# Kernel optimization log

Hardware: AMD Instinct MI355X
Metric: run time of the kernel (lower is better)

Reference implementation:

```python
import jax, jax.numpy as jnp
import numpy as np

H = 200
W = 200
SH = 2.0  # h / h_meters = 200/100
SW = 2.0
THRESH = 0.05   # opacity prune threshold
CHUNK = 128     # gaussians per scan step
EPS_T = 1e-4    # 3DGS transmittance early-stop
ALPHA_MIN = 1.0 / 255.0


def _rasterize(means3D, colors, opac, cov3D):
    """Orthographic BEV 3D-Gaussian-splat rasterization for one sample.
    means3D (N,3), colors (N,d), opac (N,1), cov3D (N,6) packed [xx,xy,xz,yy,yz,zz].
    Returns (d, H, W) image. Depth is identically 0 under the BEV view matrix,
    so compositing order is the input order (stable), matching the CUDA sort.
    """
    N, d = colors.shape
    P = H * W
    # pixel centers, row-major flatten: p = y*W + x
    gy, gx = jnp.meshgrid(jnp.arange(H, dtype=jnp.float32),
                          jnp.arange(W, dtype=jnp.float32), indexing='ij')
    pxf = gx.reshape(-1)
    pyf = gy.reshape(-1)

    # project means with full_proj_transform: u = -sh*y + H/2, v = -sw*x + W/2
    u = -SH * means3D[:, 1] + H / 2.0
    v = -SW * means3D[:, 0] + W / 2.0

    # 2D covariance: W2 @ Cov3D @ W2^T + 0.3*I with W2 = [[0,sh,0],[sw,0,0]]
    a = SH * SH * cov3D[:, 3] + 0.3   # var along image x (from Sigma_yy)
    c = SW * SW * cov3D[:, 0] + 0.3   # var along image y (from Sigma_xx)
    b = SH * SW * cov3D[:, 1]
    det = a * c - b * b
    valid = det > 0.0
    det_s = jnp.where(valid, det, 1.0)
    conA = c / det_s
    conB = b / det_s   # power uses +conB*dx*dy (conic.y = -b/det in CUDA)
    conC = a / det_s

    # fold pruning mask (opacity threshold) and validity into opacity
    op = jnp.where((opac[:, 0] > THRESH) & valid, opac[:, 0], 0.0)

    K = N // CHUNK
    chunks = tuple(t.reshape(K, CHUNK, *t.shape[1:])
                   for t in (u, v, conA, conB, conC, op, colors))

    def body(carry, ch):
        img, T = carry  # img (P,d), T (P,)
        u_, v_, A_, B_, C_, op_, col_ = ch
        dx = u_[:, None] - pxf[None, :]          # (C,P)
        dy = v_[:, None] - pyf[None, :]
        power = -0.5 * (A_[:, None] * dx * dx + C_[:, None] * dy * dy) \
                + B_[:, None] * dx * dy
        alpha = jnp.minimum(0.99, op_[:, None] * jnp.exp(jnp.minimum(power, 0.0)))
        # CUDA skips power>0 and alpha < 1/255
        alpha = jnp.where((power > 0.0) | (alpha < ALPHA_MIN), 0.0, alpha)
        # early termination: skip gaussian i (and all after) once T would drop < 1e-4
        T_incl = T[None, :] * jnp.cumprod(1.0 - alpha, axis=0)
        alpha = jnp.where(T_incl < EPS_T, 0.0, alpha)
        cp = jnp.cumprod(1.0 - alpha, axis=0)    # inclusive products
        T_excl = jnp.concatenate([jnp.ones((1, P), dtype=cp.dtype), cp[:-1]], axis=0)
        wgt = alpha * T_excl * T[None, :]        # (C,P)
        img = img + jnp.einsum('cp,cd->pd', wgt, col_)
        T = T * cp[-1]
        return (img, T), None

    img0 = jnp.zeros((P, d), dtype=colors.dtype)
    T0 = jnp.ones((P,), dtype=colors.dtype)
    (img, T), _ = jax.lax.scan(body, (img0, T0), chunks)
    # background is zeros -> no bg term; reshape to (d, H, W)
    return img.reshape(H, W, d).transpose(2, 0, 1)


def setup_inputs() -> dict:
    key = jax.random.key(0)
    k1, k2, k3, k4 = jax.random.split(key, 4)
    B, N, D = 2, 1024, 32
    features = jax.random.normal(k1, (B, N, D), dtype=jnp.float32)
    # BEV covers +/-50m; scale positions so most gaussians land on the canvas
    means3D = jax.random.normal(k2, (B, N, 3), dtype=jnp.float32) * 20.0
    cov3D = jax.random.uniform(k3, (B, N, 6), dtype=jnp.float32)
    opacities = jax.random.uniform(k4, (B, N, 1), dtype=jnp.float32)
    return {"features": features, "means3D": means3D,
            "cov3D": cov3D, "opacities": opacities}


def reference(features, means3D, cov3D, opacities):
    bev = jax.vmap(_rasterize)(means3D, features, opacities, cov3D)  # (B,d,H,W)
    mask = opacities[..., 0] > THRESH
    mean_count = mask.astype(jnp.float32).sum(axis=1).mean()
    return bev, mean_count
```

## Files before the change

kernel.cpp:

```cpp
#include <hip/hip_runtime.h>


#define HH 200
#define WW 200
#define DD 32
#define NG 1024
#define BB 2
#define TOTG (BB*NG)
#define OUT_IMG (BB*DD*HH*WW)


__global__ __launch_bounds__(256) void prepass_kernel(
    const float* __restrict__ means,
    const float* __restrict__ cov,
    const float* __restrict__ opac,
    float* __restrict__ ws,
    float* __restrict__ out)
{
    const int g = blockIdx.x * 256 + threadIdx.x;
    if (g < TOTG) {
        float o   = opac[g];
        float cxx = cov[g*6+0], cxy = cov[g*6+1], cyy = cov[g*6+3];
        float a   = 4.f*cyy + 0.3f;
        float cc  = 4.f*cxx + 0.3f;
        float bb  = 4.f*cxy;
        float det = a*cc - bb*bb;
        float u=0.f, v=0.f, A=0.f, Bc=0.f, Cc=0.f, pl=0.f, r=-1.f;
        if (o > 0.05f && det > 0.f) {
            float inv = 1.f/det;
            A = cc*inv; Bc = bb*inv; Cc = a*inv;
            float mx = means[g*3+0], my = means[g*3+1];
            u = -2.f*my + 100.f;
            v = -2.f*mx + 100.f;
            pl = -__logf(255.f*o);
            float qmax = -2.f*pl;
            float htr = 0.5f*(A+Cc), hdf = 0.5f*(A-Cc);
            float lmin = htr - sqrtf(hdf*hdf + Bc*Bc);
            r = sqrtf(qmax/lmin) + 0.5f;
        }
        ws[0*TOTG+g]=u;  ws[1*TOTG+g]=v;  ws[2*TOTG+g]=A;  ws[3*TOTG+g]=Bc;
        ws[4*TOTG+g]=Cc; ws[5*TOTG+g]=o;  ws[6*TOTG+g]=pl; ws[7*TOTG+g]=r;
    }
    if (blockIdx.x == 0) {
        const int tid = threadIdx.x;
        float s = 0.f;
        for (int i = tid; i < TOTG; i += 256)
            s += (opac[i] > 0.05f) ? 1.f : 0.f;
#pragma unroll
        for (int off = 32; off > 0; off >>= 1)
            s += __shfl_down(s, off, 64);
        __shared__ float wsum[4];
        if ((tid & 63) == 0) wsum[tid >> 6] = s;
        __syncthreads();
        if (tid == 0)
            out[OUT_IMG] = (wsum[0]+wsum[1]+wsum[2]+wsum[3]) / (float)BB;
    }
}

__global__ __launch_bounds__(64) void render_kernel(
    const float* __restrict__ feats,
    const float* __restrict__ ws,
    float* __restrict__ out)
{
    __shared__ float su[64], sv[64], sA[64], sB[64], sC[64], sop[64], spl[64];
    __shared__ int   sg[64];

    const int b    = blockIdx.z;
    const int lane = threadIdx.x;
    const int px   = blockIdx.x*8 + (lane & 7);
    const int py   = blockIdx.y*8 + (lane >> 3);
    const float pxf = (float)px, pyf = (float)py;
    const float cx  = blockIdx.x*8 + 3.5f;
    const float cy  = blockIdx.y*8 + 3.5f;

    const float* __restrict__ featsB = feats + (size_t)b * NG * DD;
    const int gbase = b * NG;

    float4 acc[8];
#pragma unroll
    for (int j = 0; j < 8; ++j) acc[j] = make_float4(0.f,0.f,0.f,0.f);
    float T = 1.f, P = 1.f;
    bool skip = false;

    for (int k = 0; k < NG/64; ++k) {
        const int g = gbase + k*64 + lane;
        const float u = ws[0*TOTG+g];
        const float v = ws[1*TOTG+g];
        const float r = ws[7*TOTG+g];
        const bool flag = (r > 0.f) &&
                          (fabsf(u - cx) <= 3.5f + r) &&
                          (fabsf(v - cy) <= 3.5f + r);
        const unsigned long long mask = __ballot(flag);
        const int m = (int)__popcll(mask);
        __syncthreads();
        if (flag) {
            const int pos = (int)__popcll(mask & ((1ull << lane) - 1ull));
            su[pos]=u; sv[pos]=v;
            sA[pos]=ws[2*TOTG+g]; sB[pos]=ws[3*TOTG+g]; sC[pos]=ws[4*TOTG+g];
            sop[pos]=ws[5*TOTG+g]; spl[pos]=ws[6*TOTG+g];
            sg[pos]=k*64 + lane;
        }
        __syncthreads();

        if (!skip) {
            for (int i = 0; i < m; ++i) {
                const float dx = su[i] - pxf;
                const float dy = sv[i] - pyf;
                const float pw = fmaf(sB[i], dx*dy,
                                      -0.5f*(sA[i]*dx*dx + sC[i]*dy*dy));
                if (pw > 0.f) continue;
                if (pw < spl[i] - 1e-3f) continue;
                const float alpha = fminf(0.99f, sop[i] * __expf(pw));
                if (alpha < (1.f/255.f)) continue;
                const float om = 1.f - alpha;
                const float tp = T * P;
                if (tp * om < 1e-4f) { skip = true; break; }
                const float w = alpha * tp;
                const float4* __restrict__ col =
                    (const float4*)(featsB + (size_t)sg[i] * DD);
#pragma unroll
                for (int j = 0; j < 8; ++j) {
                    const float4 c4 = col[j];
                    acc[j].x = fmaf(w, c4.x, acc[j].x);
                    acc[j].y = fmaf(w, c4.y, acc[j].y);
                    acc[j].z = fmaf(w, c4.z, acc[j].z);
                    acc[j].w = fmaf(w, c4.w, acc[j].w);
                }
                P *= om;
            }
        }
        if (k & 1) {
            T *= P; P = 1.f; skip = false;
            if (__ballot(T >= 1e-4f) == 0ull) break;
        }
    }

    const size_t base = (size_t)b * DD * (HH*WW) + (size_t)py * WW + px;
#pragma unroll
    for (int j = 0; j < 8; ++j) {
        out[base + (size_t)(4*j+0)*(HH*WW)] = acc[j].x;
        out[base + (size_t)(4*j+1)*(HH*WW)] = acc[j].y;
        out[base + (size_t)(4*j+2)*(HH*WW)] = acc[j].z;
        out[base + (size_t)(4*j+3)*(HH*WW)] = acc[j].w;
    }
}

extern "C" void kernel_launch(void* const* d_in, const int* in_sizes, int n_in,
                              void* d_out, int out_size, void* d_ws, size_t ws_size,
                              hipStream_t stream) {
    const float* feats = (const float*)d_in[0];
    const float* means = (const float*)d_in[1];
    const float* cvr   = (const float*)d_in[2];
    const float* opc   = (const float*)d_in[3];
    float* out = (float*)d_out;
    float* wsf = (float*)d_ws;

    prepass_kernel<<<dim3(TOTG/256), dim3(256), 0, stream>>>(means, cvr, opc, wsf, out);
    render_kernel<<<dim3(WW/8, HH/8, BB), dim3(64), 0, stream>>>(feats, wsf, out);
}
```

Measured before the change: 86.54 us.

## Split gaussian list across four waves per tile and fuse prepass into render

```diff
diff --git a/kernel.cpp b/kernel.cpp
--- a/kernel.cpp
+++ b/kernel.cpp
@@ -6,67 +6,29 @@
 #define DD 32
 #define NG 1024
 #define BB 2
-#define TOTG (BB*NG)
 #define OUT_IMG (BB*DD*HH*WW)
+#define NW 4
+#define SEGG (NG/NW)
+#define NGRP (SEGG/64)
 
-
-__global__ __launch_bounds__(256) void prepass_kernel(
+__global__ __launch_bounds__(64*NW) void render_kernel(
+    const float* __restrict__ feats,
     const float* __restrict__ means,
     const float* __restrict__ cov,
     const float* __restrict__ opac,
-    float* __restrict__ ws,
     float* __restrict__ out)
 {
-    const int g = blockIdx.x * 256 + threadIdx.x;
-    if (g < TOTG) {
-        float o   = opac[g];
-        float cxx = cov[g*6+0], cxy = cov[g*6+1], cyy = cov[g*6+3];
-        float a   = 4.f*cyy + 0.3f;
-        float cc  = 4.f*cxx + 0.3f;
-        float bb  = 4.f*cxy;
-        float det = a*cc - bb*bb;
-        float u=0.f, v=0.f, A=0.f, Bc=0.f, Cc=0.f, pl=0.f, r=-1.f;
-        if (o > 0.05f && det > 0.f) {
-            float inv = 1.f/det;
-            A = cc*inv; Bc = bb*inv; Cc = a*inv;
-            float mx = means[g*3+0], my = means[g*3+1];
-            u = -2.f*my + 100.f;
-            v = -2.f*mx + 100.f;
-            pl = -__logf(255.f*o);
-            float qmax = -2.f*pl;
-            float htr = 0.5f*(A+Cc), hdf = 0.5f*(A-Cc);
-            float lmin = htr - sqrtf(hdf*hdf + Bc*Bc);
-            r = sqrtf(qmax/lmin) + 0.5f;
-        }
-        ws[0*TOTG+g]=u;  ws[1*TOTG+g]=v;  ws[2*TOTG+g]=A;  ws[3*TOTG+g]=Bc;
-        ws[4*TOTG+g]=Cc; ws[5*TOTG+g]=o;  ws[6*TOTG+g]=pl; ws[7*TOTG+g]=r;
-    }
-    if (blockIdx.x == 0) {
-        const int tid = threadIdx.x;
-        float s = 0.f;
-        for (int i = tid; i < TOTG; i += 256)
-            s += (opac[i] > 0.05f) ? 1.f : 0.f;
-#pragma unroll
-        for (int off = 32; off > 0; off >>= 1)
-            s += __shfl_down(s, off, 64);
-        __shared__ float wsum[4];
-        if ((tid & 63) == 0) wsum[tid >> 6] = s;
-        __syncthreads();
-        if (tid == 0)
-            out[OUT_IMG] = (wsum[0]+wsum[1]+wsum[2]+wsum[3]) / (float)BB;
-    }
-}
-
-__global__ __launch_bounds__(64) void render_kernel(
-    const float* __restrict__ feats,
-    const float* __restrict__ ws,
-    float* __restrict__ out)
-{
-    __shared__ float su[64], sv[64], sA[64], sB[64], sC[64], sop[64], spl[64];
-    __shared__ int   sg[64];
+    __shared__ float su[NW][64], sv[NW][64], sA[NW][64], sB[NW][64],
+                     sC[NW][64], sop[NW][64], spl[NW][64];
+    __shared__ int   sg[NW][64];
+    __shared__ float4 simg[NW][64][8];
+    __shared__ float sT[NW][64];
+    __shared__ float wsum[NW];
 
     const int b    = blockIdx.z;
-    const int lane = threadIdx.x;
+    const int tid  = threadIdx.x;
+    const int lane = tid & 63;
+    const int wid  = tid >> 6;
     const int px   = blockIdx.x*8 + (lane & 7);
     const int py   = blockIdx.y*8 + (lane >> 3);
     const float pxf = (float)px, pyf = (float)py;
@@ -74,7 +36,7 @@
     const float cy  = blockIdx.y*8 + 3.5f;
 
     const float* __restrict__ featsB = feats + (size_t)b * NG * DD;
-    const int gbase = b * NG;
+    const int gB = b * NG;
 
     float4 acc[8];
 #pragma unroll
@@ -82,42 +44,55 @@
     float T = 1.f, P = 1.f;
     bool skip = false;
 
-    for (int k = 0; k < NG/64; ++k) {
-        const int g = gbase + k*64 + lane;
-        const float u = ws[0*TOTG+g];
-        const float v = ws[1*TOTG+g];
-        const float r = ws[7*TOTG+g];
-        const bool flag = (r > 0.f) &&
-                          (fabsf(u - cx) <= 3.5f + r) &&
-                          (fabsf(v - cy) <= 3.5f + r);
+    for (int k = 0; k < NGRP; ++k) {
+        const int gl = wid*SEGG + k*64 + lane;
+        const int g  = gB + gl;
+        const float o  = opac[g];
+        const float c0 = cov[g*6+0], c1 = cov[g*6+1], c3 = cov[g*6+3];
+        const float av = 4.f*c3 + 0.3f;
+        const float cv = 4.f*c0 + 0.3f;
+        const float bv = 4.f*c1;
+        const float det = av*cv - bv*bv;
+        bool flag = false;
+        float u=0.f, v=0.f, A=0.f, Bc=0.f, Cc=0.f, pl=0.f;
+        if (o > 0.05f && det > 0.f) {
+            const float inv = 1.f/det;
+            A = cv*inv; Bc = bv*inv; Cc = av*inv;
+            u = -2.f*means[g*3+1] + 100.f;
+            v = -2.f*means[g*3+0] + 100.f;
+            pl = -__logf(255.f*o);
+            const float qmax = -2.f*pl;
+            const float htr = 0.5f*(A+Cc), hdf = 0.5f*(A-Cc);
+            const float lmin = htr - sqrtf(hdf*hdf + Bc*Bc);
+            const float r = sqrtf(qmax/lmin) + 0.5f;
+            flag = (fabsf(u - cx) <= 3.5f + r) && (fabsf(v - cy) <= 3.5f + r);
+        }
         const unsigned long long mask = __ballot(flag);
         const int m = (int)__popcll(mask);
         __syncthreads();
         if (flag) {
             const int pos = (int)__popcll(mask & ((1ull << lane) - 1ull));
-            su[pos]=u; sv[pos]=v;
-            sA[pos]=ws[2*TOTG+g]; sB[pos]=ws[3*TOTG+g]; sC[pos]=ws[4*TOTG+g];
-            sop[pos]=ws[5*TOTG+g]; spl[pos]=ws[6*TOTG+g];
-            sg[pos]=k*64 + lane;
+            su[wid][pos]=u;  sv[wid][pos]=v;  sA[wid][pos]=A;  sB[wid][pos]=Bc;
+            sC[wid][pos]=Cc; sop[wid][pos]=o; spl[wid][pos]=pl; sg[wid][pos]=gl;
         }
         __syncthreads();
 
         if (!skip) {
             for (int i = 0; i < m; ++i) {
-                const float dx = su[i] - pxf;
-                const float dy = sv[i] - pyf;
-                const float pw = fmaf(sB[i], dx*dy,
-                                      -0.5f*(sA[i]*dx*dx + sC[i]*dy*dy));
+                const float dx = su[wid][i] - pxf;
+                const float dy = sv[wid][i] - pyf;
+                const float pw = fmaf(sB[wid][i], dx*dy,
+                                      -0.5f*(sA[wid][i]*dx*dx + sC[wid][i]*dy*dy));
                 if (pw > 0.f) continue;
-                if (pw < spl[i] - 1e-3f) continue;
-                const float alpha = fminf(0.99f, sop[i] * __expf(pw));
+                if (pw < spl[wid][i] - 1e-3f) continue;
+                const float alpha = fminf(0.99f, sop[wid][i] * __expf(pw));
                 if (alpha < (1.f/255.f)) continue;
                 const float om = 1.f - alpha;
                 const float tp = T * P;
                 if (tp * om < 1e-4f) { skip = true; break; }
                 const float w = alpha * tp;
                 const float4* __restrict__ col =
-                    (const float4*)(featsB + (size_t)sg[i] * DD);
+                    (const float4*)(featsB + (size_t)sg[wid][i] * DD);
 #pragma unroll
                 for (int j = 0; j < 8; ++j) {
                     const float4 c4 = col[j];
@@ -129,19 +104,54 @@
                 P *= om;
             }
         }
-        if (k & 1) {
-            T *= P; P = 1.f; skip = false;
-            if (__ballot(T >= 1e-4f) == 0ull) break;
+        if (k & 1) { T *= P; P = 1.f; skip = false; }
+    }
+
+    sT[wid][lane] = T;
+#pragma unroll
+    for (int j = 0; j < 8; ++j)
+        simg[wid][lane][(j + lane) & 7] = acc[j];
+    __syncthreads();
+
+    {
+        const int p   = tid & 63;
+        const int grp = tid >> 6;
+        const float t0 = sT[0][p], t1 = sT[1][p], t2 = sT[2][p];
+        const float pf1 = t0, pf2 = t0*t1, pf3 = pf2*t2;
+        const int ppx = blockIdx.x*8 + (p & 7);
+        const int ppy = blockIdx.y*8 + (p >> 3);
+        const size_t base = (size_t)b * DD * (HH*WW) + (size_t)ppy * WW + ppx;
+#pragma unroll
+        for (int q = 0; q < 2; ++q) {
+            const int c4 = grp*2 + q;
+            const int slot = (c4 + p) & 7;
+            const float4 r0 = simg[0][p][slot];
+            const float4 r1 = simg[1][p][slot];
+            const float4 r2 = simg[2][p][slot];
+            const float4 r3 = simg[3][p][slot];
+            float4 ov;
+            ov.x = fmaf(pf3, r3.x, fmaf(pf2, r2.x, fmaf(pf1, r1.x, r0.x)));
+            ov.y = fmaf(pf3, r3.y, fmaf(pf2, r2.y, fmaf(pf1, r1.y, r0.y)));
+            ov.z = fmaf(pf3, r3.z, fmaf(pf2, r2.z, fmaf(pf1, r1.z, r0.z)));
+            ov.w = fmaf(pf3, r3.w, fmaf(pf2, r2.w, fmaf(pf1, r1.w, r0.w)));
+            out[base + (size_t)(c4*4+0)*(HH*WW)] = ov.x;
+            out[base + (size_t)(c4*4+1)*(HH*WW)] = ov.y;
+            out[base + (size_t)(c4*4+2)*(HH*WW)] = ov.z;
+            out[base + (size_t)(c4*4+3)*(HH*WW)] = ov.w;
         }
     }
 
-    const size_t base = (size_t)b * DD * (HH*WW) + (size_t)py * WW + px;
+    if (blockIdx.x == 0 && blockIdx.y == 0 && b == 0) {
+        float s = 0.f;
+        for (int i = tid; i < BB*NG; i += 64*NW)
+            s += (opac[i] > 0.05f) ? 1.f : 0.f;
 #pragma unroll
-    for (int j = 0; j < 8; ++j) {
-        out[base + (size_t)(4*j+0)*(HH*WW)] = acc[j].x;
-        out[base + (size_t)(4*j+1)*(HH*WW)] = acc[j].y;
-        out[base + (size_t)(4*j+2)*(HH*WW)] = acc[j].z;
-        out[base + (size_t)(4*j+3)*(HH*WW)] = acc[j].w;
+        for (int off = 32; off > 0; off >>= 1)
+            s += __shfl_down(s, off, 64);
+        if (lane == 0) wsum[wid] = s;
+        __syncthreads();
+        if (tid == 0)
+            out[OUT_IMG] = (wsum[0]+wsum[1]+wsum[2]+wsum[3]) * (1.f/(float)BB);
     }
 }
 
@@ -153,8 +163,7 @@
     const float* cvr   = (const float*)d_in[2];
     const float* opc   = (const float*)d_in[3];
     float* out = (float*)d_out;
-    float* wsf = (float*)d_ws;
 
-    prepass_kernel<<<dim3(TOTG/256), dim3(256), 0, stream>>>(means, cvr, opc, wsf, out);
-    render_kernel<<<dim3(WW/8, HH/8, BB), dim3(64), 0, stream>>>(feats, wsf, out);
+    render_kernel<<<dim3(WW/8, HH/8, BB), dim3(64*NW), 0, stream>>>(
+        feats, means, cvr, opc, out);
 }
```

After: 77.47 us. 10.5% less time.
